# Performance work log

Measured on AMD Instinct MI355X. Metric: run time of the kernel, lower is better.

The kernel has to match this reference:

```python
import jax, jax.numpy as jnp
import numpy as np

B, S, H, NH = 2, 2048, 1024, 16
D = H // NH


def setup_inputs() -> dict:
    key = jax.random.key(0)
    ks = jax.random.split(key, 7)
    scale = 1.0 / np.sqrt(H)
    return {
        "x": jax.random.normal(ks[0], (B, S, H), dtype=jnp.float32),
        "Wq": jax.random.normal(ks[1], (H, H), dtype=jnp.float32) * scale,
        "bq": jax.random.normal(ks[2], (H,), dtype=jnp.float32) * 0.01,
        "Wk": jax.random.normal(ks[3], (H, H), dtype=jnp.float32) * scale,
        "bk": jax.random.normal(ks[4], (H,), dtype=jnp.float32) * 0.01,
        "Wv": jax.random.normal(ks[5], (H, H), dtype=jnp.float32) * scale,
        "bv": jax.random.normal(ks[6], (H,), dtype=jnp.float32) * 0.01,
    }


def reference(x, Wq, bq, Wk, bk, Wv, bv):
    b, s, h = x.shape
    n, d = NH, h // NH
    # QKV projections (torch Linear: x @ W.T + b)
    q = (x @ Wq.T + bq).reshape(b, s, n, d).transpose(0, 2, 1, 3)  # [b,n,s,d]
    k = (x @ Wk.T + bk).reshape(b, s, n, d).transpose(0, 2, 1, 3)
    v = (x @ Wv.T + bv).reshape(b, s, n, d).transpose(0, 2, 1, 3)
    # NOTE: original module applies NO 1/sqrt(d) scaling -- stay faithful.
    scores = jnp.einsum("bnqd,bnkd->bnqk", q, k)  # [b,n,s,s]
    probs = jax.nn.softmax(scores, axis=-1)
    attn = jnp.einsum("bnqk,bnkd->bnqd", probs, v)  # [b,n,s,d]
    return attn.transpose(0, 2, 1, 3).reshape(b, s, h)
```

## Files before the change

### kernel.cpp

```cpp
#include <hip/hip_runtime.h>
#include <hip/hip_bf16.h>

typedef unsigned int uint;
typedef unsigned short ushort;
typedef _Float16 f16;
typedef __attribute__((ext_vector_type(4))) float f32x4;
typedef __attribute__((ext_vector_type(8))) _Float16 f16x8;
typedef __attribute__((ext_vector_type(8))) ushort ushort8;

#define MFMAH(a, b, c) __builtin_amdgcn_mfma_f32_16x16x32_f16((a), (b), (c), 0, 0, 0)

#if __has_builtin(__builtin_amdgcn_permlane32_swap) && __has_builtin(__builtin_amdgcn_permlane16_swap)
#define HAVE_PERMLANE_SWAP 1
#else
#define HAVE_PERMLANE_SWAP 0
#endif

__device__ __forceinline__ float exp2_raw(float x) {
    return __builtin_amdgcn_exp2f(x);
}

__device__ __forceinline__ ushort f2h(float x) {
    f16 h = (f16)x;
    return __builtin_bit_cast(ushort, h);
}
__device__ __forceinline__ uint pk_f16(float lo, float hi) {
    auto t = __builtin_amdgcn_cvt_pkrtz(lo, hi);
    return __builtin_bit_cast(uint, t);
}

__device__ __forceinline__ void gload_lds16(const void* g, void* l) {
    __builtin_amdgcn_global_load_lds(
        (const __attribute__((address_space(1))) void*)g,
        (__attribute__((address_space(3))) void*)l, 16, 0, 0);
}

__global__ __launch_bounds__(256) void cvt_all(const float* __restrict__ x,
                                               const float* __restrict__ Wq,
                                               const float* __restrict__ Wk,
                                               const float* __restrict__ Wv,
                                               ushort* __restrict__ xf,
                                               ushort* __restrict__ wf) {
    const int blk = blockIdx.x;
    const float* src;
    ushort* dst;
    int i;
    if (blk < 2048) {
        src = x;  dst = xf;              i = blk * 256 + threadIdx.x;
    } else if (blk < 2560) {
        src = Wq; dst = wf;              i = (blk - 2048) * 256 + threadIdx.x;
    } else if (blk < 3072) {
        src = Wk; dst = wf + 1024 * 1024; i = (blk - 2560) * 256 + threadIdx.x;
    } else {
        src = Wv; dst = wf + 2 * 1024 * 1024; i = (blk - 3072) * 256 + threadIdx.x;
    }
    const float4* s4 = reinterpret_cast<const float4*>(src);
    float4 a = s4[2 * i], b = s4[2 * i + 1];
    float v[8] = {a.x, a.y, a.z, a.w, b.x, b.y, b.z, b.w};
    ushort8 o;
#pragma unroll
    for (int j = 0; j < 8; ++j) o[j] = f2h(v[j]);
    *reinterpret_cast<ushort8*>(dst + i * 8) = o;
}

__global__ __launch_bounds__(256, 3) void qkv_gemm(const ushort* __restrict__ xf,
                                                   const ushort* __restrict__ wf,
                                                   const float* __restrict__ bq,
                                                   const float* __restrict__ bk,
                                                   const float* __restrict__ bv,
                                                   ushort* __restrict__ qh,
                                                   ushort* __restrict__ kh,
                                                   ushort* __restrict__ vt) {
    __shared__ ushort Asf[128 * 64];
    __shared__ ushort Bsf[128 * 64];
    const int tid = threadIdx.x;
    const int l = tid & 63, w = tid >> 6;
    const int lrow = l & 15, lhi = l >> 4;
    const int wr = w >> 1, wc = w & 1;
    const int m0 = blockIdx.x * 128;
    const int n0 = blockIdx.y * 128;
    const int z = blockIdx.z;
    const ushort* wz = wf + z * (1024 * 1024);
    const float* bias = (z == 0) ? bq : (z == 1) ? bk : bv;

    f32x4 acc[4][4] = {};
    const int srow = w * 32 + (l >> 3);
    const int scol = ((l & 7) ^ (l >> 3)) * 8;
    const int lds0 = w * 2048;
    const int arow = wr * 64 + lrow;
    const int brow = wc * 64 + lrow;

    for (int kt = 0; kt < 16; ++kt) {
        const int kb = kt * 64;
#pragma unroll
        for (int i = 0; i < 4; ++i) {
            gload_lds16(xf + (m0 + srow + i * 8) * 1024 + kb + scol, &Asf[lds0 + i * 512]);
            gload_lds16(wz + (n0 + srow + i * 8) * 1024 + kb + scol, &Bsf[lds0 + i * 512]);
        }
        __syncthreads();
#pragma unroll
        for (int kk = 0; kk < 2; ++kk) {
            const int csw = ((kk * 4 + lhi) ^ (lrow & 7)) * 8;
            f16x8 axf[4];
#pragma unroll
            for (int mi = 0; mi < 4; ++mi)
                axf[mi] = *reinterpret_cast<const f16x8*>(&Asf[(arow + mi * 16) * 64 + csw]);
            __builtin_amdgcn_s_setprio(1);
#pragma unroll
            for (int ni = 0; ni < 4; ++ni) {
                f16x8 bf8 = *reinterpret_cast<const f16x8*>(&Bsf[(brow + ni * 16) * 64 + csw]);
#pragma unroll
                for (int mi = 0; mi < 4; ++mi)
                    acc[mi][ni] = MFMAH(axf[mi], bf8, acc[mi][ni]);
            }
            __builtin_amdgcn_s_setprio(0);
        }
        __syncthreads();
    }
    float bcol[4];
#pragma unroll
    for (int ni = 0; ni < 4; ++ni) bcol[ni] = bias[n0 + wc * 64 + ni * 16 + lrow];
    if (z == 2) {
#pragma unroll
        for (int mi = 0; mi < 4; ++mi) {
            const int m = m0 + wr * 64 + mi * 16 + lhi * 4;
            const int bb = m >> 11, s = m & 2047;
#pragma unroll
            for (int ni = 0; ni < 4; ++ni) {
                const int n = n0 + wc * 64 + ni * 16 + lrow;
                const int h = n >> 6, d = n & 63;
                ushort4 pk4;
                pk4.x = f2h(acc[mi][ni][0] + bcol[ni]);
                pk4.y = f2h(acc[mi][ni][1] + bcol[ni]);
                pk4.z = f2h(acc[mi][ni][2] + bcol[ni]);
                pk4.w = f2h(acc[mi][ni][3] + bcol[ni]);
                *reinterpret_cast<ushort4*>(vt + ((size_t)(bb * 16 + h) * 64 + d) * 2048 + s) = pk4;
            }
        }
    } else {
        const float qscale = (z == 0) ? 1.4426950408889634f : 1.0f;
        ushort* dst = (z == 0) ? qh : kh;
#pragma unroll
        for (int mi = 0; mi < 4; ++mi) {
#pragma unroll
            for (int r = 0; r < 4; ++r) {
                const int m = m0 + wr * 64 + mi * 16 + lhi * 4 + r;
                const int bb = m >> 11, s = m & 2047;
#pragma unroll
                for (int ni = 0; ni < 4; ++ni) {
                    const int n = n0 + wc * 64 + ni * 16 + lrow;
                    const int h = n >> 6, d = n & 63;
                    dst[((bb * 16 + h) * 2048 + s) * 64 + d] =
                        f2h((acc[mi][ni][r] + bcol[ni]) * qscale);
                }
            }
        }
    }
}

__global__ __launch_bounds__(512, 4) void attn_fwd(const ushort* __restrict__ Qhg,
                                                   const ushort* __restrict__ Khg,
                                                   const ushort* __restrict__ Vtg,
                                                   float* __restrict__ out) {
    __shared__ ushort Ksh[2][64 * 64];
    __shared__ ushort Vts[2][64 * 64];
    const int tid = threadIdx.x;
    const int l = tid & 63, w = tid >> 6;
    const int lrow = l & 15, lhi = l >> 4;
    const int wsub = w & 3;
    const int qt = blockIdx.x * 2 + (w >> 2);
    const int bh = blockIdx.y;
    const int b = bh >> 4, h = bh & 15;
    const size_t qoff = ((size_t)bh * 2048 + qt * 64) * 64;
    const size_t kvoff = (size_t)bh * 2048 * 64;
    const size_t vtoff = (size_t)bh * 64 * 2048;

    f16x8 aqh[2];
#pragma unroll
    for (int kk = 0; kk < 2; ++kk) {
        const size_t qa = qoff + (wsub * 16 + lrow) * 64 + kk * 32 + lhi * 8;
        aqh[kk] = *reinterpret_cast<const f16x8*>(Qhg + qa);
    }

    const f16x8 ones = {(f16)1, (f16)1, (f16)1, (f16)1, (f16)1, (f16)1, (f16)1, (f16)1};

    const int srow = w * 8 + (l >> 3);
    const int scol = ((l & 7) ^ (l >> 3)) * 8;
    const int lds0 = w * 512;

    const int bl = (lhi << 4) + lhi * 4;

    float m_run = 0.f;
    f32x4 o[4];
    f32x4 l_acc = f32x4{0.f, 0.f, 0.f, 0.f};
#pragma unroll
    for (int ni = 0; ni < 4; ++ni) o[ni] = f32x4{0.f, 0.f, 0.f, 0.f};

    auto stage = [&](int buf, int t) {
        const size_t gk = kvoff + (size_t)(t * 64 + srow) * 64 + scol;
        const size_t gv = vtoff + (size_t)srow * 2048 + t * 64 + scol;
        gload_lds16(Khg + gk, &Ksh[buf][lds0]);
        gload_lds16(Vtg + gv, &Vts[buf][lds0]);
    };

    auto tilecomp = [&](int buf) {
        f32x4 sc[4];
        const f32x4 minit = {-m_run, -m_run, -m_run, -m_run};
#pragma unroll
        for (int ni = 0; ni < 4; ++ni) sc[ni] = minit;
        __builtin_amdgcn_s_setprio(1);
#pragma unroll
        for (int kk = 0; kk < 2; ++kk) {
#pragma unroll
            for (int ni = 0; ni < 4; ++ni) {
                const int off = (ni * 16 + lrow) * 64 + (((kk * 4 + lhi) ^ (lrow & 7)) * 8);
                f16x8 khf = *reinterpret_cast<const f16x8*>(&Ksh[buf][off]);
                sc[ni] = MFMAH(khf, aqh[kk], sc[ni]);
            }
        }
        __builtin_amdgcn_s_setprio(0);

        float mx = fmaxf(fmaxf(sc[0][0], sc[0][1]), sc[0][2]);
        mx = fmaxf(fmaxf(mx, sc[0][3]), sc[1][0]);
        mx = fmaxf(fmaxf(mx, sc[1][1]), sc[1][2]);
        mx = fmaxf(fmaxf(mx, sc[1][3]), sc[2][0]);
        mx = fmaxf(fmaxf(mx, sc[2][1]), sc[2][2]);
        mx = fmaxf(fmaxf(mx, sc[2][3]), sc[3][0]);
        mx = fmaxf(fmaxf(mx, sc[3][1]), sc[3][2]);
        mx = fmaxf(mx, sc[3][3]);
        mx = fmaxf(mx, __shfl_xor(mx, 16, 64));
        mx = fmaxf(mx, __shfl_xor(mx, 32, 64));

        float p[4][4];
        if (__any(mx > 8.f)) {
            const float delta = fmaxf(mx, 0.f);
            m_run += delta;
            const float alpha = exp2_raw(-delta);
#pragma unroll
            for (int ni = 0; ni < 4; ++ni)
#pragma unroll
                for (int rr = 0; rr < 4; ++rr)
                    p[ni][rr] = exp2_raw(sc[ni][rr] - delta);
            float ao0 = __shfl(alpha, bl + 0, 64);
            float ao1 = __shfl(alpha, bl + 1, 64);
            float ao2 = __shfl(alpha, bl + 2, 64);
            float ao3 = __shfl(alpha, bl + 3, 64);
#pragma unroll
            for (int ni = 0; ni < 4; ++ni) {
                o[ni][0] *= ao0; o[ni][1] *= ao1; o[ni][2] *= ao2; o[ni][3] *= ao3;
            }
            l_acc[0] *= ao0; l_acc[1] *= ao1; l_acc[2] *= ao2; l_acc[3] *= ao3;
        } else {
#pragma unroll
            for (int ni = 0; ni < 4; ++ni)
#pragma unroll
                for (int rr = 0; rr < 4; ++rr)
                    p[ni][rr] = exp2_raw(sc[ni][rr]);
        }
        uint pk[4][2];
#pragma unroll
        for (int ni = 0; ni < 4; ++ni) {
            pk[ni][0] = pk_f16(p[ni][0], p[ni][1]);
            pk[ni][1] = pk_f16(p[ni][2], p[ni][3]);
        }
        uint apw[2][4];
#if HAVE_PERMLANE_SWAP
#pragma unroll
        for (int kk = 0; kk < 2; ++kk) {
#pragma unroll
            for (int c = 0; c < 2; ++c) {
                auto r1 = __builtin_amdgcn_permlane32_swap(pk[2 * kk][c], pk[2 * kk + 1][c],
                                                           false, false);
                auto r2 = __builtin_amdgcn_permlane16_swap(r1[0], r1[1], false, false);
                apw[kk][c]     = (uint)r2[0];
                apw[kk][2 + c] = (uint)r2[1];
            }
        }
#else
        const int s0 = lrow + 32 * (lhi & 1);
        const int s1 = s0 + 16;
        const bool abit = (lhi >> 1) != 0;
#pragma unroll
        for (int kk = 0; kk < 2; ++kk) {
            int t0, t1;
            t0 = __shfl((int)pk[2 * kk][0], s0, 64); t1 = __shfl((int)pk[2 * kk + 1][0], s0, 64);
            apw[kk][0] = (uint)(abit ? t1 : t0);
            t0 = __shfl((int)pk[2 * kk][1], s0, 64); t1 = __shfl((int)pk[2 * kk + 1][1], s0, 64);
            apw[kk][1] = (uint)(abit ? t1 : t0);
            t0 = __shfl((int)pk[2 * kk][0], s1, 64); t1 = __shfl((int)pk[2 * kk + 1][0], s1, 64);
            apw[kk][2] = (uint)(abit ? t1 : t0);
            t0 = __shfl((int)pk[2 * kk][1], s1, 64); t1 = __shfl((int)pk[2 * kk + 1][1], s1, 64);
            apw[kk][3] = (uint)(abit ? t1 : t0);
        }
#endif
        __builtin_amdgcn_s_setprio(1);
#pragma unroll
        for (int kk = 0; kk < 2; ++kk) {
            f16x8 ap = *reinterpret_cast<const f16x8*>(&apw[kk][0]);
#pragma unroll
            for (int ni = 0; ni < 4; ++ni) {
                const int off = (ni * 16 + lrow) * 64 + (((kk * 4 + lhi) ^ (lrow & 7)) * 8);
                f16x8 vf = *reinterpret_cast<const f16x8*>(&Vts[buf][off]);
                o[ni] = MFMAH(ap, vf, o[ni]);
            }
            l_acc = MFMAH(ap, ones, l_acc);
        }
        __builtin_amdgcn_s_setprio(0);
    };

    stage(0, 0);
    __syncthreads();
#pragma unroll 1
    for (int tt = 0; tt < 16; ++tt) {
        stage(1, tt * 2 + 1);
        tilecomp(0);
        __syncthreads();
        if (tt < 15) stage(0, tt * 2 + 2);
        tilecomp(1);
        __syncthreads();
    }

    const float inv0 = 1.f / l_acc[0];
    const float inv1 = 1.f / l_acc[1];
    const float inv2 = 1.f / l_acc[2];
    const float inv3 = 1.f / l_acc[3];
#pragma unroll
    for (int ni = 0; ni < 4; ++ni) {
        const int q = qt * 64 + wsub * 16 + lhi * 4;
        const int d = ni * 16 + lrow;
        float* op = out + ((size_t)b * 2048 + q) * 1024 + h * 64 + d;
        op[0]        = o[ni][0] * inv0;
        op[1024]     = o[ni][1] * inv1;
        op[2 * 1024] = o[ni][2] * inv2;
        op[3 * 1024] = o[ni][3] * inv3;
    }
}

extern "C" void kernel_launch(void* const* d_in, const int* in_sizes, int n_in,
                              void* d_out, int out_size, void* d_ws, size_t ws_size,
                              hipStream_t stream) {
    const float* x  = (const float*)d_in[0];
    const float* Wq = (const float*)d_in[1];
    const float* bq = (const float*)d_in[2];
    const float* Wk = (const float*)d_in[3];
    const float* bk = (const float*)d_in[4];
    const float* Wv = (const float*)d_in[5];
    const float* bv = (const float*)d_in[6];
    float* outp = (float*)d_out;

    ushort* ws = (ushort*)d_ws;
    const size_t XM = 4096 * 1024;
    const size_t WM = 1024 * 1024;
    ushort* xf = ws;
    ushort* wf = xf + XM;
    ushort* qh = wf + 3 * WM;
    ushort* kh = qh + XM;
    ushort* vt = kh + XM;

    cvt_all<<<3584, 256, 0, stream>>>(x, Wq, Wk, Wv, xf, wf);

    qkv_gemm<<<dim3(32, 8, 3), 256, 0, stream>>>(xf, wf, bq, bk, bv, qh, kh, vt);

    attn_fwd<<<dim3(16, 32), 512, 0, stream>>>(qh, kh, vt, outp);
}
```

Measured before the change: 94.05 us.

## Process two KV tiles per iteration with quad-buffered LDS and batched QK

Doubles the LDS K/V buffers to four and stages two KV tiles ahead per iteration. Both QK^T MFMA blocks are issued back to back before the softmax/PV of each, giving more independent MFMA work to overlap with the exp and shuffle latency. It also halves the number of barriers. The second tile's softmax compensates for the max update made by the first tile through a pending offset. LDS use doubles, to 64KB per block, and register pressure rises, which may reduce occupancy below the launch bound target.

```diff
diff --git a/kernel.cpp b/kernel.cpp
--- a/kernel.cpp
+++ b/kernel.cpp
@@ -162,8 +162,8 @@
                                                    const ushort* __restrict__ Khg,
                                                    const ushort* __restrict__ Vtg,
                                                    float* __restrict__ out) {
-    __shared__ ushort Ksh[2][64 * 64];
-    __shared__ ushort Vts[2][64 * 64];
+    __shared__ ushort Ksh[4][64 * 64];
+    __shared__ ushort Vts[4][64 * 64];
     const int tid = threadIdx.x;
     const int l = tid & 63, w = tid >> 6;
     const int lrow = l & 15, lhi = l >> 4;
@@ -203,8 +203,7 @@
         gload_lds16(Vtg + gv, &Vts[buf][lds0]);
     };
 
-    auto tilecomp = [&](int buf) {
-        f32x4 sc[4];
+    auto qk = [&](int buf, f32x4* sc) {
         const f32x4 minit = {-m_run, -m_run, -m_run, -m_run};
 #pragma unroll
         for (int ni = 0; ni < 4; ++ni) sc[ni] = minit;
@@ -219,7 +218,9 @@
             }
         }
         __builtin_amdgcn_s_setprio(0);
-
+    };
+
+    auto smpv = [&](f32x4* sc, int buf, float pend, bool pendnz) -> float {
         float mx = fmaxf(fmaxf(sc[0][0], sc[0][1]), sc[0][2]);
         mx = fmaxf(fmaxf(mx, sc[0][3]), sc[1][0]);
         mx = fmaxf(fmaxf(mx, sc[1][1]), sc[1][2]);
@@ -231,16 +232,19 @@
         mx = fmaxf(mx, __shfl_xor(mx, 16, 64));
         mx = fmaxf(mx, __shfl_xor(mx, 32, 64));
 
+        const float mrel = mx - pend;
         float p[4][4];
-        if (__any(mx > 8.f)) {
-            const float delta = fmaxf(mx, 0.f);
+        float delta = 0.f;
+        if (__any(mrel > 8.f)) {
+            delta = fmaxf(mrel, 0.f);
             m_run += delta;
+            const float shift = pend + delta;
             const float alpha = exp2_raw(-delta);
 #pragma unroll
             for (int ni = 0; ni < 4; ++ni)
 #pragma unroll
                 for (int rr = 0; rr < 4; ++rr)
-                    p[ni][rr] = exp2_raw(sc[ni][rr] - delta);
+                    p[ni][rr] = exp2_raw(sc[ni][rr] - shift);
             float ao0 = __shfl(alpha, bl + 0, 64);
             float ao1 = __shfl(alpha, bl + 1, 64);
             float ao2 = __shfl(alpha, bl + 2, 64);
@@ -250,6 +254,12 @@
                 o[ni][0] *= ao0; o[ni][1] *= ao1; o[ni][2] *= ao2; o[ni][3] *= ao3;
             }
             l_acc[0] *= ao0; l_acc[1] *= ao1; l_acc[2] *= ao2; l_acc[3] *= ao3;
+        } else if (pendnz) {
+#pragma unroll
+            for (int ni = 0; ni < 4; ++ni)
+#pragma unroll
+                for (int rr = 0; rr < 4; ++rr)
+                    p[ni][rr] = exp2_raw(sc[ni][rr] - pend);
         } else {
 #pragma unroll
             for (int ni = 0; ni < 4; ++ni)
@@ -306,17 +316,26 @@
             l_acc = MFMAH(ap, ones, l_acc);
         }
         __builtin_amdgcn_s_setprio(0);
+        return delta;
     };
 
     stage(0, 0);
+    stage(1, 1);
     __syncthreads();
 #pragma unroll 1
-    for (int tt = 0; tt < 16; ++tt) {
-        stage(1, tt * 2 + 1);
-        tilecomp(0);
-        __syncthreads();
-        if (tt < 15) stage(0, tt * 2 + 2);
-        tilecomp(1);
+    for (int pp = 0; pp < 16; ++pp) {
+        const int ba = (pp & 1) * 2;
+        const int nb = ((pp + 1) & 1) * 2;
+        if (pp < 15) {
+            stage(nb, 2 * pp + 2);
+            stage(nb + 1, 2 * pp + 3);
+        }
+        f32x4 sca[4], scb[4];
+        qk(ba, sca);
+        qk(ba + 1, scb);
+        float da = smpv(sca, ba, 0.f, false);
+        bool an = __any(da != 0.f);
+        smpv(scb, ba + 1, da, an);
         __syncthreads();
     }
 
```

Result: no change. 95.23 us (+1.3%).
